# Kernel optimization log

Measured on AMD Instinct MI355X. Metric: run time of the kernel, lower is better.

Reference implementation:

```python
import jax, jax.numpy as jnp
import numpy as np

N, C, DFF, TMAX = 4, 768, 3072, 20
RMS_EPS = 1e-6
SINK_EPS = 1e-6
POST_MULT = 2.0


def setup_inputs() -> dict:
    key = jax.random.key(0)
    ks = jax.random.split(key, 5)
    B, S = 4, 4096
    x = jax.random.normal(ks[0], (B, S, N, C), dtype=jnp.float32)
    phi = jax.random.normal(ks[1], (N * C, N * N + 2 * N), dtype=jnp.float32) * 0.02
    b = jnp.zeros((N * N + 2 * N,), dtype=jnp.float32)
    alpha_pre = jnp.ones((1,), dtype=jnp.float32)
    alpha_post = jnp.ones((1,), dtype=jnp.float32)
    alpha_res = jnp.ones((1,), dtype=jnp.float32)
    W1 = jax.random.normal(ks[2], (C, DFF), dtype=jnp.float32) * (1.0 / np.sqrt(C))
    b1 = jnp.zeros((DFF,), dtype=jnp.float32)
    W2 = jax.random.normal(ks[3], (DFF, C), dtype=jnp.float32) * (1.0 / np.sqrt(DFF))
    b2 = jnp.zeros((C,), dtype=jnp.float32)
    return {"x": x, "phi": phi, "b": b, "alpha_pre": alpha_pre,
            "alpha_post": alpha_post, "alpha_res": alpha_res,
            "W1": W1, "b1": b1, "W2": W2, "b2": b2}


def _sinkhorn(logits):
    # logits: (..., 16) -> doubly-stochastic (..., 4, 4); rows = logits[..., 4i:4i+4]
    r = logits.reshape(*logits.shape[:-1], N, N)
    r = jnp.exp(r - jnp.max(r, axis=-1, keepdims=True))
    for _ in range(TMAX):
        r = r / (jnp.sum(r, axis=-1, keepdims=True) + SINK_EPS)  # row normalize
        r = r / (jnp.sum(r, axis=-2, keepdims=True) + SINK_EPS)  # column normalize
    return r


def _mhc_forward(x, phi, b, alpha_pre, alpha_post, alpha_res, W1, b1, W2, b2):
    lead = x.shape[:-2]
    x_mat = x.reshape(-1, N * C)
    # fused RMS-norm + linear routing projection
    invr = jax.lax.rsqrt(jnp.mean(x_mat * x_mat, axis=-1, keepdims=True) + RMS_EPS)
    mix = (x_mat @ phi) * invr  # (T, n^2 + 2n)
    h_pre = jax.nn.sigmoid(mix[:, :N] * alpha_pre + b[:N]).reshape(*lead, N)
    h_post = (jax.nn.sigmoid(mix[:, N:2 * N] * alpha_post + b[N:2 * N]) * POST_MULT).reshape(*lead, N)
    h_res = _sinkhorn(mix[:, 2 * N:] * alpha_res + b[2 * N:]).reshape(*lead, N, N)
    # pre-aggregate n streams -> single full-width stream
    x_in = jnp.einsum('...nc,...n->...c', x, h_pre)
    # wrapped sublayer: baseline MLP at full width
    f_out = jax.nn.gelu(x_in @ W1 + b1, approximate=False) @ W2 + b2
    # residual stream mixing + post scatter
    res_gather = jnp.einsum('...ij,...jc->...ic', h_res, x)
    return res_gather + h_post[..., None] * f_out[..., None, :]


def reference(x, phi, b, alpha_pre, alpha_post, alpha_res, W1, b1, W2, b2):
    return _mhc_forward(x, phi, b, alpha_pre, alpha_post, alpha_res, W1, b1, W2, b2)
```

## Files before the change

kernel.cpp:

```cpp
#include <hip/hip_runtime.h>
#include <hip/hip_bf16.h>
#include <stdint.h>

#define NT   16384
#define C_   768
#define DFF_ 3072
#define KX   3072
#define NMIX 24
#define TB   64
#define KSPLIT 4
#define KSEG (KX / KSPLIT)

typedef __attribute__((ext_vector_type(8))) short shortx8;
typedef __attribute__((ext_vector_type(4))) float floatx4;

__device__ __forceinline__ short f2bf(float f) {
  union { float f; uint32_t u; } v; v.f = f;
  uint32_t r = v.u + 0x7fffu + ((v.u >> 16) & 1u);
  return (short)(r >> 16);
}

__device__ __forceinline__ float bf2f(short s) {
  union { uint32_t u; float f; } v;
  v.u = ((uint32_t)(uint16_t)s) << 16;
  return v.f;
}

__device__ __forceinline__ float gelu_f(float v) {
  float u = 1.5957691216057308f * v * (1.0f + 0.044715f * v * v);
  return v / (1.0f + __expf(-u));
}

__global__ void phiT_kernel(const float* __restrict__ phi, float* __restrict__ phiT) {
  int idx = blockIdx.x * 256 + threadIdx.x;
  if (idx < KX * NMIX) {
    int k = idx / NMIX, j = idx - k * NMIX;
    phiT[(size_t)j * KX + k] = phi[idx];
  }
}

__global__ __launch_bounds__(256) void transpose_bf16(const float* __restrict__ in,
                                                      short* __restrict__ out,
                                                      int R, int C) {
  __shared__ float tile[32][33];
  int bx = blockIdx.x * 32;
  int by = blockIdx.y * 32;
  int tx = threadIdx.x & 31, ty = threadIdx.x >> 5;
  #pragma unroll
  for (int i = 0; i < 32; i += 8)
    tile[ty + i][tx] = in[(size_t)(by + ty + i) * C + bx + tx];
  __syncthreads();
  #pragma unroll
  for (int i = 0; i < 32; i += 8)
    out[(size_t)(bx + ty + i) * R + by + tx] = f2bf(tile[tx][ty + i]);
}

__global__ __launch_bounds__(256) void k1a(
    const float* __restrict__ x, const float* __restrict__ phiT,
    float* __restrict__ pmix, float* __restrict__ pssq) {
  __shared__ float xs[TB][132];
  int tid = threadIdx.x;
  int lane = tid & 63;
  int w = tid >> 6;
  int wu = __builtin_amdgcn_readfirstlane(w);
  int t0 = (blockIdx.x >> 2) * TB;
  int slot = blockIdx.x & 3;
  int ks = slot * KSEG;

  float acc[6] = {0.f, 0.f, 0.f, 0.f, 0.f, 0.f};
  float ssq = 0.f;

  for (int kc = ks; kc < ks + KSEG; kc += 128) {
    if (kc != ks) __syncthreads();
    #pragma unroll
    for (int jj = 0; jj < 8; ++jj) {
      int idx = tid + jj * 256;
      int row = idx >> 5, c4 = idx & 31;
      const float4 v = *(const float4*)&x[(size_t)(t0 + row) * KX + kc + c4 * 4];
      *(float4*)&xs[row][c4 * 4] = v;
    }
    __syncthreads();
    #pragma unroll 4
    for (int k4 = 0; k4 < 32; ++k4) {
      const float4 xv = *(const float4*)&xs[lane][k4 * 4];
      if (w == 0) ssq += xv.x * xv.x + xv.y * xv.y + xv.z * xv.z + xv.w * xv.w;
      int kk = kc + k4 * 4;
      #pragma unroll
      for (int jj = 0; jj < 6; ++jj) {
        const float4 p = *(const float4*)&phiT[(size_t)(wu * 6 + jj) * KX + kk];
        acc[jj] += p.x * xv.x + p.y * xv.y + p.z * xv.z + p.w * xv.w;
      }
    }
  }
  if (w == 0) pssq[(size_t)(t0 + lane) * KSPLIT + slot] = ssq;
  #pragma unroll
  for (int jj = 0; jj < 6; ++jj)
    pmix[((size_t)(t0 + lane) * KSPLIT + slot) * NMIX + wu * 6 + jj] = acc[jj];
}

__global__ __launch_bounds__(256) void k1b(
    const float* __restrict__ pmix, const float* __restrict__ pssq,
    const float* __restrict__ bvec, const float* __restrict__ a_pre,
    const float* __restrict__ a_post, const float* __restrict__ a_res,
    float* __restrict__ hpre, float* __restrict__ hpost, float* __restrict__ hres) {
  __shared__ float mixs[TB][NMIX];
  __shared__ float invr_s[TB];
  int tid = threadIdx.x;
  int t0 = blockIdx.x * TB;
  int tq = tid >> 2, r = tid & 3;

  {
    const float* pm = pmix + (size_t)(t0 + tq) * KSPLIT * NMIX;
    float s[6] = {0.f, 0.f, 0.f, 0.f, 0.f, 0.f};
    #pragma unroll
    for (int sl = 0; sl < KSPLIT; ++sl)
      #pragma unroll
      for (int jj = 0; jj < 6; ++jj)
        s[jj] += pm[sl * NMIX + r * 6 + jj];
    #pragma unroll
    for (int jj = 0; jj < 6; ++jj) mixs[tq][r * 6 + jj] = s[jj];
    if (r == 0) {
      const float* ps = pssq + (size_t)(t0 + tq) * KSPLIT;
      float sq = ps[0] + ps[1] + ps[2] + ps[3];
      invr_s[tq] = rsqrtf(sq * (1.0f / KX) + 1e-6f);
    }
  }
  __syncthreads();

  {
    float invr = invr_s[tq];
    float ares = a_res[0];
    float v0 = mixs[tq][8 + r * 4 + 0] * invr * ares + bvec[8 + r * 4 + 0];
    float v1 = mixs[tq][8 + r * 4 + 1] * invr * ares + bvec[8 + r * 4 + 1];
    float v2 = mixs[tq][8 + r * 4 + 2] * invr * ares + bvec[8 + r * 4 + 2];
    float v3 = mixs[tq][8 + r * 4 + 3] * invr * ares + bvec[8 + r * 4 + 3];
    float mx = fmaxf(fmaxf(v0, v1), fmaxf(v2, v3));
    v0 = __expf(v0 - mx); v1 = __expf(v1 - mx); v2 = __expf(v2 - mx); v3 = __expf(v3 - mx);
    for (int it = 0; it < 20; ++it) {
      float s = v0 + v1 + v2 + v3 + 1e-6f;
      float inv = 1.0f / s;
      v0 *= inv; v1 *= inv; v2 *= inv; v3 *= inv;
      float c0 = v0 + __shfl_xor(v0, 1); c0 += __shfl_xor(c0, 2);
      float c1 = v1 + __shfl_xor(v1, 1); c1 += __shfl_xor(c1, 2);
      float c2 = v2 + __shfl_xor(v2, 1); c2 += __shfl_xor(c2, 2);
      float c3 = v3 + __shfl_xor(v3, 1); c3 += __shfl_xor(c3, 2);
      v0 /= (c0 + 1e-6f); v1 /= (c1 + 1e-6f); v2 /= (c2 + 1e-6f); v3 /= (c3 + 1e-6f);
    }
    float* ho = hres + (size_t)(t0 + tq) * 16 + r * 4;
    ho[0] = v0; ho[1] = v1; ho[2] = v2; ho[3] = v3;
    if (r == 0) {
      float apre = a_pre[0];
      float4 hp;
      hp.x = 1.0f / (1.0f + __expf(-(mixs[tq][0] * invr * apre + bvec[0])));
      hp.y = 1.0f / (1.0f + __expf(-(mixs[tq][1] * invr * apre + bvec[1])));
      hp.z = 1.0f / (1.0f + __expf(-(mixs[tq][2] * invr * apre + bvec[2])));
      hp.w = 1.0f / (1.0f + __expf(-(mixs[tq][3] * invr * apre + bvec[3])));
      *(float4*)&hpre[(size_t)(t0 + tq) * 4] = hp;
    } else if (r == 1) {
      float apost = a_post[0];
      float4 hq;
      hq.x = 2.0f / (1.0f + __expf(-(mixs[tq][4] * invr * apost + bvec[4])));
      hq.y = 2.0f / (1.0f + __expf(-(mixs[tq][5] * invr * apost + bvec[5])));
      hq.z = 2.0f / (1.0f + __expf(-(mixs[tq][6] * invr * apost + bvec[6])));
      hq.w = 2.0f / (1.0f + __expf(-(mixs[tq][7] * invr * apost + bvec[7])));
      *(float4*)&hpost[(size_t)(t0 + tq) * 4] = hq;
    }
  }
}

__global__ __launch_bounds__(256) void k1c(
    const float* __restrict__ x, const float* __restrict__ hpre,
    short* __restrict__ x_in) {
  int idx = blockIdx.x * 256 + threadIdx.x;
  int t = idx / 192;
  int c = (idx - t * 192) * 4;
  float4 hp = *(const float4*)&hpre[(size_t)t * 4];
  const float* xr = x + (size_t)t * KX + c;
  float4 x0 = *(const float4*)(xr);
  float4 x1 = *(const float4*)(xr + C_);
  float4 x2 = *(const float4*)(xr + 2 * C_);
  float4 x3 = *(const float4*)(xr + 3 * C_);
  short4 s;
  s.x = f2bf(hp.x * x0.x + hp.y * x1.x + hp.z * x2.x + hp.w * x3.x);
  s.y = f2bf(hp.x * x0.y + hp.y * x1.y + hp.z * x2.y + hp.w * x3.y);
  s.z = f2bf(hp.x * x0.z + hp.y * x1.z + hp.z * x2.z + hp.w * x3.z);
  s.w = f2bf(hp.x * x0.w + hp.y * x1.w + hp.z * x2.w + hp.w * x3.w);
  *(short4*)&x_in[(size_t)t * C_ + c] = s;
}

template <int EPI>
__global__ __launch_bounds__(256, 3) void gemm_bt(
    const short* __restrict__ A, const short* __restrict__ B,
    int M, int N, int K, const float* __restrict__ bias,
    short* __restrict__ outb,
    const float* __restrict__ x, const float* __restrict__ hres,
    const float* __restrict__ hpost, float* __restrict__ out) {
  __shared__ short As[128 * 32];
  __shared__ short Bs[128 * 32];
  __shared__ __align__(16) short cb[128 * 136];
  int tid = threadIdx.x;
  int lane = tid & 63, w = tid >> 6;
  int m0 = blockIdx.y * 128, n0 = blockIdx.x * 128;
  int wm = (w >> 1) * 64, wn = (w & 1) * 64;
  int lrow = lane & 15, quad = lane >> 4;
  floatx4 acc[4][4] = {};

  for (int k0 = 0; k0 < K; k0 += 32) {
    if (k0) __syncthreads();
    #pragma unroll
    for (int i = 0; i < 2; ++i) {
      int c = tid + i * 256;
      int row = c >> 2, slot = c & 3;
      const short* ga = A + (size_t)(m0 + row) * K + k0 + slot * 8;
      const short* gb = B + (size_t)(n0 + row) * K + k0 + slot * 8;
      __builtin_amdgcn_global_load_lds((const __attribute__((address_space(1))) void*)ga,
                                       (__attribute__((address_space(3))) void*)&As[c * 8],
                                       16, 0, 0);
      __builtin_amdgcn_global_load_lds((const __attribute__((address_space(1))) void*)gb,
                                       (__attribute__((address_space(3))) void*)&Bs[c * 8],
                                       16, 0, 0);
    }
    __syncthreads();
    shortx8 af[4], bfr[4];
    #pragma unroll
    for (int mi = 0; mi < 4; ++mi)
      af[mi] = *(const shortx8*)&As[(wm + mi * 16 + lrow) * 32 + quad * 8];
    #pragma unroll
    for (int ni = 0; ni < 4; ++ni)
      bfr[ni] = *(const shortx8*)&Bs[(wn + ni * 16 + lrow) * 32 + quad * 8];
    #pragma unroll
    for (int mi = 0; mi < 4; ++mi)
      #pragma unroll
      for (int ni = 0; ni < 4; ++ni)
        acc[mi][ni] = __builtin_amdgcn_mfma_f32_16x16x32_bf16(af[mi], bfr[ni], acc[mi][ni], 0, 0, 0);
  }

  float bcol[4];
  #pragma unroll
  for (int ni = 0; ni < 4; ++ni) bcol[ni] = bias[n0 + wn + ni * 16 + lrow];

  #pragma unroll
  for (int mi = 0; mi < 4; ++mi) {
    #pragma unroll
    for (int r = 0; r < 4; ++r) {
      int rr = wm + mi * 16 + quad * 4 + r;
      #pragma unroll
      for (int ni = 0; ni < 4; ++ni) {
        int col = wn + ni * 16 + lrow;
        float v = acc[mi][ni][r] + bcol[ni];
        if (EPI == 1) v = gelu_f(v);
        cb[rr * 136 + col] = f2bf(v);
      }
    }
  }
  __syncthreads();

  int rbase = tid >> 4, ic = tid & 15;
  if (EPI == 1) {
    #pragma unroll
    for (int v = 0; v < 8; ++v) {
      int rr = v * 16 + rbase;
      shortx8 val = *(const shortx8*)&cb[rr * 136 + ic * 8];
      *(shortx8*)&outb[(size_t)(m0 + rr) * N + n0 + ic * 8] = val;
    }
  } else {
    #pragma unroll
    for (int v = 0; v < 8; ++v) {
      int rr = v * 16 + rbase;
      int tr = m0 + rr;
      shortx8 f8 = *(const shortx8*)&cb[rr * 136 + ic * 8];
      float fv[8];
      #pragma unroll
      for (int j = 0; j < 8; ++j) fv[j] = bf2f(f8[j]);
      const float* xr = x + (size_t)tr * KX + n0 + ic * 8;
      float4 xa[4], xb[4];
      #pragma unroll
      for (int n = 0; n < 4; ++n) {
        xa[n] = *(const float4*)(xr + n * 768);
        xb[n] = *(const float4*)(xr + n * 768 + 4);
      }
      const float4* hrp = (const float4*)(hres + (size_t)tr * 16);
      float4 hp4 = *(const float4*)&hpost[(size_t)tr * 4];
      float hpv[4] = {hp4.x, hp4.y, hp4.z, hp4.w};
      float* orow = out + (size_t)tr * KX + n0 + ic * 8;
      #pragma unroll
      for (int n = 0; n < 4; ++n) {
        float4 h = hrp[n];
        float4 oa, ob;
        oa.x = h.x * xa[0].x + h.y * xa[1].x + h.z * xa[2].x + h.w * xa[3].x + hpv[n] * fv[0];
        oa.y = h.x * xa[0].y + h.y * xa[1].y + h.z * xa[2].y + h.w * xa[3].y + hpv[n] * fv[1];
        oa.z = h.x * xa[0].z + h.y * xa[1].z + h.z * xa[2].z + h.w * xa[3].z + hpv[n] * fv[2];
        oa.w = h.x * xa[0].w + h.y * xa[1].w + h.z * xa[2].w + h.w * xa[3].w + hpv[n] * fv[3];
        ob.x = h.x * xb[0].x + h.y * xb[1].x + h.z * xb[2].x + h.w * xb[3].x + hpv[n] * fv[4];
        ob.y = h.x * xb[0].y + h.y * xb[1].y + h.z * xb[2].y + h.w * xb[3].y + hpv[n] * fv[5];
        ob.z = h.x * xb[0].z + h.y * xb[1].z + h.z * xb[2].z + h.w * xb[3].z + hpv[n] * fv[6];
        ob.w = h.x * xb[0].w + h.y * xb[1].w + h.z * xb[2].w + h.w * xb[3].w + hpv[n] * fv[7];
        *(float4*)(orow + n * 768) = oa;
        *(float4*)(orow + n * 768 + 4) = ob;
      }
    }
  }
}

extern "C" void kernel_launch(void* const* d_in, const int* in_sizes, int n_in,
                              void* d_out, int out_size, void* d_ws, size_t ws_size,
                              hipStream_t stream) {
  const float* x      = (const float*)d_in[0];
  const float* phi    = (const float*)d_in[1];
  const float* b      = (const float*)d_in[2];
  const float* a_pre  = (const float*)d_in[3];
  const float* a_post = (const float*)d_in[4];
  const float* a_res  = (const float*)d_in[5];
  const float* W1     = (const float*)d_in[6];
  const float* b1     = (const float*)d_in[7];
  const float* W2     = (const float*)d_in[8];
  const float* b2     = (const float*)d_in[9];
  float* out = (float*)d_out;

  char* ws = (char*)d_ws;
  size_t off = 0;
  auto carve = [&](size_t bytes) {
    char* p = ws + off;
    off += (bytes + 255) & ~(size_t)255;
    return p;
  };
  short* x_in  = (short*)carve((size_t)NT * C_ * 2);
  short* act   = (short*)carve((size_t)NT * DFF_ * 2);
  float* hpost = (float*)carve((size_t)NT * 4 * 4);
  float* hres  = (float*)carve((size_t)NT * 16 * 4);
  float* hpre  = (float*)carve((size_t)NT * 4 * 4);
  short* W1T   = (short*)carve((size_t)DFF_ * C_ * 2);
  short* W2T   = (short*)carve((size_t)C_ * DFF_ * 2);
  float* phiT  = (float*)carve((size_t)NMIX * KX * 4);
  float* pmix  = (float*)carve((size_t)NT * KSPLIT * NMIX * 4);
  float* pssq  = (float*)carve((size_t)NT * KSPLIT * 4);

  phiT_kernel<<<dim3((KX * NMIX + 255) / 256), 256, 0, stream>>>(phi, phiT);
  transpose_bf16<<<dim3(DFF_ / 32, C_ / 32), 256, 0, stream>>>(W1, W1T, C_, DFF_);
  transpose_bf16<<<dim3(C_ / 32, DFF_ / 32), 256, 0, stream>>>(W2, W2T, DFF_, C_);
  k1a<<<dim3((NT / TB) * KSPLIT), 256, 0, stream>>>(x, phiT, pmix, pssq);
  k1b<<<dim3(NT / TB), 256, 0, stream>>>(pmix, pssq, b, a_pre, a_post, a_res,
                                         hpre, hpost, hres);
  k1c<<<dim3(NT * 192 / 256), 256, 0, stream>>>(x, hpre, x_in);
  gemm_bt<1><<<dim3(DFF_ / 128, NT / 128), 256, 0, stream>>>(
      x_in, W1T, NT, DFF_, C_, b1, act, nullptr, nullptr, nullptr, nullptr);
  gemm_bt<2><<<dim3(C_ / 128, NT / 128), 256, 0, stream>>>(
      act, W2T, NT, C_, DFF_, b2, nullptr, x, hres, hpost, out);
}
```

Before: 705.6 us.

## Double-buffer GEMM LDS tiles, swizzle block order across XCDs, alias epilogue LDS

```diff
diff --git a/kernel.cpp b/kernel.cpp
--- a/kernel.cpp
+++ b/kernel.cpp
@@ -195,44 +195,59 @@
     short* __restrict__ outb,
     const float* __restrict__ x, const float* __restrict__ hres,
     const float* __restrict__ hpost, float* __restrict__ out) {
-  __shared__ short As[128 * 32];
-  __shared__ short Bs[128 * 32];
-  __shared__ __align__(16) short cb[128 * 136];
+  __shared__ __align__(16) char smem[34816];
+  short* As = (short*)smem;
+  short* Bs = (short*)(smem + 16384);
+  short* cb = (short*)smem;
   int tid = threadIdx.x;
   int lane = tid & 63, w = tid >> 6;
-  int m0 = blockIdx.y * 128, n0 = blockIdx.x * 128;
+  int nwg = gridDim.x * gridDim.y;
+  int lid = blockIdx.y * gridDim.x + blockIdx.x;
+  int sid = (lid & 7) * (nwg >> 3) + (lid >> 3);
+  int bx = sid % gridDim.x, by = sid / gridDim.x;
+  int m0 = by * 128, n0 = bx * 128;
   int wm = (w >> 1) * 64, wn = (w & 1) * 64;
   int lrow = lane & 15, quad = lane >> 4;
   floatx4 acc[4][4] = {};
 
-  for (int k0 = 0; k0 < K; k0 += 32) {
-    if (k0) __syncthreads();
-    #pragma unroll
-    for (int i = 0; i < 2; ++i) {
-      int c = tid + i * 256;
-      int row = c >> 2, slot = c & 3;
-      const short* ga = A + (size_t)(m0 + row) * K + k0 + slot * 8;
-      const short* gb = B + (size_t)(n0 + row) * K + k0 + slot * 8;
-      __builtin_amdgcn_global_load_lds((const __attribute__((address_space(1))) void*)ga,
-                                       (__attribute__((address_space(3))) void*)&As[c * 8],
-                                       16, 0, 0);
-      __builtin_amdgcn_global_load_lds((const __attribute__((address_space(1))) void*)gb,
-                                       (__attribute__((address_space(3))) void*)&Bs[c * 8],
-                                       16, 0, 0);
-    }
-    __syncthreads();
+  int srow = tid >> 2, sslot = tid & 3;
+  int srow2 = (tid + 256) >> 2, sslot2 = (tid + 256) & 3;
+
+  auto stage = [&](int buf, int k0) {
+    const short* ga = A + (size_t)(m0 + srow) * K + k0 + sslot * 8;
+    const short* gb = B + (size_t)(n0 + srow) * K + k0 + sslot * 8;
+    __builtin_amdgcn_global_load_lds((const __attribute__((address_space(1))) void*)ga,
+        (__attribute__((address_space(3))) void*)&As[buf * 4096 + tid * 8], 16, 0, 0);
+    __builtin_amdgcn_global_load_lds((const __attribute__((address_space(1))) void*)gb,
+        (__attribute__((address_space(3))) void*)&Bs[buf * 4096 + tid * 8], 16, 0, 0);
+    const short* ga2 = A + (size_t)(m0 + srow2) * K + k0 + sslot2 * 8;
+    const short* gb2 = B + (size_t)(n0 + srow2) * K + k0 + sslot2 * 8;
+    __builtin_amdgcn_global_load_lds((const __attribute__((address_space(1))) void*)ga2,
+        (__attribute__((address_space(3))) void*)&As[buf * 4096 + (tid + 256) * 8], 16, 0, 0);
+    __builtin_amdgcn_global_load_lds((const __attribute__((address_space(1))) void*)gb2,
+        (__attribute__((address_space(3))) void*)&Bs[buf * 4096 + (tid + 256) * 8], 16, 0, 0);
+  };
+
+  int ntiles = K >> 5;
+  stage(0, 0);
+  __syncthreads();
+  int cur = 0;
+  for (int t = 0; t < ntiles; ++t) {
+    if (t + 1 < ntiles) stage(cur ^ 1, (t + 1) << 5);
     shortx8 af[4], bfr[4];
     #pragma unroll
     for (int mi = 0; mi < 4; ++mi)
-      af[mi] = *(const shortx8*)&As[(wm + mi * 16 + lrow) * 32 + quad * 8];
+      af[mi] = *(const shortx8*)&As[cur * 4096 + (wm + mi * 16 + lrow) * 32 + quad * 8];
     #pragma unroll
     for (int ni = 0; ni < 4; ++ni)
-      bfr[ni] = *(const shortx8*)&Bs[(wn + ni * 16 + lrow) * 32 + quad * 8];
+      bfr[ni] = *(const shortx8*)&Bs[cur * 4096 + (wn + ni * 16 + lrow) * 32 + quad * 8];
     #pragma unroll
     for (int mi = 0; mi < 4; ++mi)
       #pragma unroll
       for (int ni = 0; ni < 4; ++ni)
         acc[mi][ni] = __builtin_amdgcn_mfma_f32_16x16x32_bf16(af[mi], bfr[ni], acc[mi][ni], 0, 0, 0);
+    __syncthreads();
+    cur ^= 1;
   }
 
   float bcol[4];
```

Result: faster. 678.9 us (-3.8%).
